# Kernel tuning notes

Measured on AMD Instinct MI355X. Metric: run time of the kernel, lower is better.

## Reference

```python
import jax, jax.numpy as jnp
import numpy as np
from functools import partial

B, T, F_DIM, H_ATT = 1024, 32, 64, 64
NUM_FILTERS, KH, KW = 64, 2, 2
CATE_SIZES = [1665, 217, 2501]  # cate_unique_num + 1
CATE_DIM = 8
NUM_CLASSES = 2
FLAT_DIM = NUM_FILTERS * (T - KH + 1) * (2 * F_DIM - KW + 1)  # 64*31*127
LIN1_IN = FLAT_DIM + 3 * CATE_DIM


def setup_inputs() -> dict:
    key = jax.random.key(0)
    ks = jax.random.split(key, 16)
    X_nume = jax.random.normal(ks[0], (B, T, F_DIM), dtype=jnp.float32)
    X_cate = jax.random.randint(ks[1], (B, 3), 0, 217, dtype=jnp.int64)
    # attention params: uniform(0,1) as in the torch module
    W_att = jax.random.uniform(ks[2], (F_DIM, H_ATT), dtype=jnp.float32)
    U_att = jax.random.uniform(ks[3], (F_DIM, H_ATT), dtype=jnp.float32)
    V_att = jax.random.uniform(ks[4], (H_ATT, 1), dtype=jnp.float32)
    conv_w = jax.random.normal(ks[5], (NUM_FILTERS, 1, KH, KW), dtype=jnp.float32) * 0.1
    conv_b = jax.random.normal(ks[6], (NUM_FILTERS,), dtype=jnp.float32) * 0.01
    emb0 = jax.random.normal(ks[7], (CATE_SIZES[0], CATE_DIM), dtype=jnp.float32)
    emb1 = jax.random.normal(ks[8], (CATE_SIZES[1], CATE_DIM), dtype=jnp.float32)
    emb2 = jax.random.normal(ks[9], (CATE_SIZES[2], CATE_DIM), dtype=jnp.float32)
    w1 = jax.random.normal(ks[10], (256, LIN1_IN), dtype=jnp.float32) * 0.002
    b1 = jnp.zeros((256,), dtype=jnp.float32)
    w2 = jax.random.normal(ks[11], (32, 256), dtype=jnp.float32) * 0.06
    b2 = jnp.zeros((32,), dtype=jnp.float32)
    w3 = jax.random.normal(ks[12], (NUM_CLASSES, 32), dtype=jnp.float32) * 0.17
    b3 = jnp.zeros((NUM_CLASSES,), dtype=jnp.float32)
    return dict(X_nume=X_nume, X_cate=X_cate, W_att=W_att, U_att=U_att, V_att=V_att,
                conv_w=conv_w, conv_b=conv_b, emb0=emb0, emb1=emb1, emb2=emb2,
                w1=w1, b1=b1, w2=w2, b2=b2, w3=w3, b3=b3)


def _forward(X_nume, X_cate, W_att, U_att, V_att, conv_w, conv_b,
             emb0, emb1, emb2, w1, b1, w2, b2, w3, b3):
    # ---- pairwise additive attention over time (GAT-style) ----
    Xw = jnp.einsum('btf,fh->bth', X_nume, W_att)  # [B,T,H]
    Xu = jnp.einsum('btf,fh->bth', X_nume, U_att)  # [B,T,H]
    h = jnp.tanh(Xw[:, :, None, :] + Xu[:, None, :, :])        # [B,T,T,H]
    e = jnp.einsum('bijh,h->bij', h, V_att[:, 0])              # [B,T,T]
    alpha = jax.nn.softmax(e, axis=2)                          # softmax over j (incl. j==i)
    # c_i = sum_{j != i} alpha_ij * x_j  (self term excluded, NOT renormalized)
    c = jnp.einsum('bij,bjf->bif', alpha, X_nume)
    alpha_diag = jnp.einsum('bii->bi', alpha)
    c = c - alpha_diag[:, :, None] * X_nume                    # [B,T,F]
    inp = jnp.concatenate([X_nume, c], axis=-1)                # [B,T,2F]
    # ---- conv 2d (1 -> num_filters, 2x2, valid) + relu ----
    conv_in = inp[:, None, :, :]                               # [B,1,T,2F]
    y = jax.lax.conv_general_dilated(conv_in, conv_w, (1, 1), 'VALID',
                                     dimension_numbers=('NCHW', 'OIHW', 'NCHW'))
    y = jax.nn.relu(y + conv_b[None, :, None, None])           # [B,64,T-1,2F-1]
    flat = y.reshape(y.shape[0], -1)
    # ---- categorical embeddings ----
    cate = jnp.concatenate([emb0[X_cate[:, 0]], emb1[X_cate[:, 1]], emb2[X_cate[:, 2]]], axis=1)
    x = jnp.concatenate([flat, cate], axis=1)
    # ---- MLP head ----
    x = jax.nn.relu(x @ w1.T + b1)
    x = jax.nn.relu(x @ w2.T + b2)
    return x @ w3.T + b3


def reference(X_nume, X_cate, W_att, U_att, V_att, conv_w, conv_b,
              emb0, emb1, emb2, w1, b1, w2, b2, w3, b3):
    return _forward(X_nume, X_cate, W_att, U_att, V_att, conv_w, conv_b,
                    emb0, emb1, emb2, w1, b1, w2, b2, w3, b3)
```

## Files before the change

### kernel.cpp

```cpp
#include <hip/hip_runtime.h>

typedef unsigned short u16;
typedef unsigned int   u32;
typedef __attribute__((ext_vector_type(4))) float f32x4;
typedef __attribute__((ext_vector_type(8))) short s16x8;
typedef __attribute__((ext_vector_type(4))) unsigned short u16x4;

#define FLATD 251968
#define LIN1  251992
#define K_    251968

__device__ __forceinline__ u16 f2bf(float f) {
  u32 u = __float_as_uint(f);
  u32 r = (u + 0x7fffu + ((u >> 16) & 1u)) >> 16;
  return (u16)r;
}

__global__ __launch_bounds__(256) void k_attn_conv(
    const float* __restrict__ Xn, const float* __restrict__ Wa,
    const float* __restrict__ Ua, const float* __restrict__ Va,
    const float* __restrict__ cw, const float* __restrict__ cb,
    u16* __restrict__ flat)
{
  __shared__ float Xs[32][65];
  __shared__ float Xw[32][65];
  __shared__ float Xu[32][65];
  __shared__ float ev[32][33];
  __shared__ float Vs[64];
  __shared__ float ins[32][132];

  const int b = blockIdx.x;
  const int t = threadIdx.x;
  const float* xb = Xn + (size_t)b * 2048;

  for (int v = t; v < 512; v += 256) {
    float4 x = ((const float4*)xb)[v];
    int row = v >> 4, c4 = (v & 15) << 2;
    Xs[row][c4] = x.x; Xs[row][c4 + 1] = x.y; Xs[row][c4 + 2] = x.z; Xs[row][c4 + 3] = x.w;
  }
  if (t < 64) Vs[t] = Va[t];
  __syncthreads();

  {
    const int h = t & 63, iw = t >> 6;
    float aw[8] = {0,0,0,0,0,0,0,0}, au[8] = {0,0,0,0,0,0,0,0};
    for (int f = 0; f < 64; ++f) {
      float wv_ = Wa[f * 64 + h], uv_ = Ua[f * 64 + h];
#pragma unroll
      for (int s = 0; s < 8; ++s) {
        float x = Xs[iw + 4 * s][f];
        aw[s] = fmaf(x, wv_, aw[s]);
        au[s] = fmaf(x, uv_, au[s]);
      }
    }
#pragma unroll
    for (int s = 0; s < 8; ++s) { Xw[iw + 4 * s][h] = aw[s]; Xu[iw + 4 * s][h] = au[s]; }
  }
  __syncthreads();

  for (int p = t; p < 1024; p += 256) {
    int i = p >> 5, j = p & 31;
    float acc = 0.f;
    for (int h = 0; h < 64; ++h) {
      float s  = Xw[i][h] + Xu[j][h];
      float ex = __expf(2.f * s);
      float th = 1.f - 2.f * __builtin_amdgcn_rcpf(ex + 1.f);
      acc = fmaf(th, Vs[h], acc);
    }
    ev[i][j] = acc;
  }
  __syncthreads();

  {
    int i = t >> 3, g = t & 7;
    float e0 = ev[i][g], e1 = ev[i][g + 8], e2 = ev[i][g + 16], e3 = ev[i][g + 24];
    float m = fmaxf(fmaxf(e0, e1), fmaxf(e2, e3));
    m = fmaxf(m, __shfl_xor(m, 1));
    m = fmaxf(m, __shfl_xor(m, 2));
    m = fmaxf(m, __shfl_xor(m, 4));
    float p0 = __expf(e0 - m), p1 = __expf(e1 - m), p2 = __expf(e2 - m), p3 = __expf(e3 - m);
    float s = p0 + p1 + p2 + p3;
    s += __shfl_xor(s, 1); s += __shfl_xor(s, 2); s += __shfl_xor(s, 4);
    float inv = __builtin_amdgcn_rcpf(s);
    ev[i][g] = p0 * inv; ev[i][g + 8] = p1 * inv; ev[i][g + 16] = p2 * inv; ev[i][g + 24] = p3 * inv;
  }
  __syncthreads();

  for (int p = t; p < 2048; p += 256) {
    int i = p >> 6, f = p & 63;
    float acc = 0.f;
#pragma unroll 8
    for (int j = 0; j < 32; ++j) acc = fmaf(ev[i][j], Xs[j][f], acc);
    acc -= ev[i][i] * Xs[i][f];
    ins[i][f]      = Xs[i][f];
    ins[i][64 + f] = acc;
  }
  __syncthreads();

  const int lane = t & 63, wv = t >> 6;
  u16* fb = flat + (size_t)b * FLATD;
  for (int fblk = 0; fblk < 8; ++fblk) {
    float w00[8], w01[8], w10[8], w11[8], bb[8];
#pragma unroll
    for (int j = 0; j < 8; ++j) {
      int f = fblk * 8 + j;
      w00[j] = cw[f * 4 + 0]; w01[j] = cw[f * 4 + 1];
      w10[j] = cw[f * 4 + 2]; w11[j] = cw[f * 4 + 3];
      bb[j]  = cb[f];
    }
    for (int s = wv; s < 62; s += 4) {
      int r = s >> 1;
      int c = ((s & 1) << 6) + lane;
      if (c < 127) {
        float x0 = ins[r][c],     x1 = ins[r][c + 1];
        float y0 = ins[r + 1][c], y1 = ins[r + 1][c + 1];
        u16* po = fb + (size_t)(fblk * 8) * 3937 + r * 127 + c;
#pragma unroll
        for (int j = 0; j < 8; ++j) {
          float y = fmaf(x0, w00[j], fmaf(x1, w01[j],
                    fmaf(y0, w10[j], fmaf(y1, w11[j], bb[j]))));
          po[(size_t)j * 3937] = f2bf(fmaxf(y, 0.f));
        }
      }
    }
  }
}

__global__ __launch_bounds__(256) void k_cast_w1(const float* __restrict__ w1,
                                                 u16* __restrict__ w1b)
{
  const int o = blockIdx.x;
  const int part = blockIdx.y;
  const int t = threadIdx.x;
  const float4* src = (const float4*)(w1 + (size_t)o * LIN1) + part * 7874;
  u16x4* dst = (u16x4*)(w1b + (size_t)o * K_) + part * 7874;
  for (int i = t; i < 7874; i += 256) {
    float4 v = src[i];
    u16x4 o4;
    o4.x = f2bf(v.x); o4.y = f2bf(v.y); o4.z = f2bf(v.z); o4.w = f2bf(v.w);
    dst[i] = o4;
  }
}

__global__ __launch_bounds__(256) void k_cate(
    const int* __restrict__ Xc, const float* __restrict__ e0,
    const float* __restrict__ e1, const float* __restrict__ e2,
    const float* __restrict__ w1, const float* __restrict__ b1,
    float* __restrict__ x1)
{
  __shared__ float es[24];
  const int b = blockIdx.x, t = threadIdx.x;
  if (t < 24) {
    int g = t >> 3, d = t & 7;
    int idx = Xc[b * 3 + g];
    const float* tab = (g == 0) ? e0 : (g == 1) ? e1 : e2;
    es[t] = tab[idx * 8 + d];
  }
  __syncthreads();
  float acc = b1[t];
  const float* wt = w1 + (size_t)t * LIN1 + FLATD;
#pragma unroll
  for (int j = 0; j < 24; ++j) acc = fmaf(es[j], wt[j], acc);
  x1[b * 256 + t] = acc;
}

#define AS1 __attribute__((address_space(1)))
#define AS3 __attribute__((address_space(3)))
__device__ __forceinline__ void g2l16(const void* g, void* l) {
  __builtin_amdgcn_global_load_lds((const AS1 u32*)g, (AS3 u32*)l, 16, 0, 0);
}

__global__ __launch_bounds__(256, 3) void k_gemm(
    const u16* __restrict__ A, const u16* __restrict__ Bw, float* __restrict__ C)
{
  __shared__ u16 As[128 * 32];
  __shared__ u16 Bs[128 * 32];
  const int tile = blockIdx.x;
  const int kc   = blockIdx.y;
  const int mt = tile & 7, nt = tile >> 3;
  const int tid = threadIdx.x;
  const int lane = tid & 63, w = tid >> 6;
  const int wm = w >> 1, wn = w & 1;

  const size_t kbase = (size_t)kc * 4064;
  const u16* gA = A  + ((size_t)(mt * 128 + w * 32 + (lane >> 2))) * K_ + kbase + (size_t)(lane & 3) * 8;
  const u16* gB = Bw + ((size_t)(nt * 128 + w * 32 + (lane >> 2))) * K_ + kbase + (size_t)(lane & 3) * 8;
  char* lA = (char*)As + w * 2048;
  char* lB = (char*)Bs + w * 2048;

  f32x4 acc[4][4] = {};

  const int aoff = (wm * 64 + (lane & 15)) * 64 + (lane >> 4) * 16;
  const int boff = (wn * 64 + (lane & 15)) * 64 + (lane >> 4) * 16;

  for (int ks = 0; ks < 127; ++ks) {
    const size_t ko = (size_t)ks * 32;
    g2l16(gA + ko,                    lA);
    g2l16(gA + ko + (size_t)16 * K_,  lA + 1024);
    g2l16(gB + ko,                    lB);
    g2l16(gB + ko + (size_t)16 * K_,  lB + 1024);
    __syncthreads();
    s16x8 af[4], bf[4];
#pragma unroll
    for (int mi = 0; mi < 4; ++mi)
      af[mi] = *(const s16x8*)((const char*)As + aoff + mi * 1024);
#pragma unroll
    for (int ni = 0; ni < 4; ++ni)
      bf[ni] = *(const s16x8*)((const char*)Bs + boff + ni * 1024);
#pragma unroll
    for (int mi = 0; mi < 4; ++mi)
#pragma unroll
      for (int ni = 0; ni < 4; ++ni)
        acc[mi][ni] = __builtin_amdgcn_mfma_f32_16x16x32_bf16(af[mi], bf[ni], acc[mi][ni], 0, 0, 0);
    __syncthreads();
  }

  const int m0 = mt * 128 + wm * 64 + ((lane >> 4) << 2);
  const int n0 = nt * 128 + wn * 64 + (lane & 15);
#pragma unroll
  for (int mi = 0; mi < 4; ++mi)
#pragma unroll
    for (int ni = 0; ni < 4; ++ni)
#pragma unroll
      for (int r = 0; r < 4; ++r)
        atomicAdd(C + (size_t)(m0 + mi * 16 + r) * 256 + (n0 + ni * 16), acc[mi][ni][r]);
}

__global__ __launch_bounds__(64) void k_tail(
    const float* __restrict__ x1, const float* __restrict__ w2, const float* __restrict__ b2,
    const float* __restrict__ w3, const float* __restrict__ b3, float* __restrict__ out)
{
  __shared__ float x2s[32];
  const int b = blockIdx.x, l = threadIdx.x;
  const int j = l & 31, og = l >> 5;
  const float* xb = x1 + b * 256 + og * 128;
  const float* wr = w2 + j * 256 + og * 128;
  float acc = 0.f;
#pragma unroll 4
  for (int i = 0; i < 128; ++i)
    acc = fmaf(fmaxf(xb[i], 0.f), wr[i], acc);
  acc += __shfl_xor(acc, 32);
  if (og == 0) x2s[j] = fmaxf(acc + b2[j], 0.f);
  __syncthreads();
  if (l < 2) {
    float r = b3[l];
#pragma unroll
    for (int q = 0; q < 32; ++q) r = fmaf(x2s[q], w3[l * 32 + q], r);
    out[(size_t)b * 2 + l] = r;
  }
}

extern "C" void kernel_launch(void* const* d_in, const int* in_sizes, int n_in,
                              void* d_out, int out_size, void* d_ws, size_t ws_size,
                              hipStream_t stream)
{
  const float* Xn = (const float*)d_in[0];
  const int*   Xc = (const int*)d_in[1];
  const float* Wa = (const float*)d_in[2];
  const float* Ua = (const float*)d_in[3];
  const float* Va = (const float*)d_in[4];
  const float* cw = (const float*)d_in[5];
  const float* cb = (const float*)d_in[6];
  const float* e0 = (const float*)d_in[7];
  const float* e1 = (const float*)d_in[8];
  const float* e2 = (const float*)d_in[9];
  const float* w1 = (const float*)d_in[10];
  const float* b1 = (const float*)d_in[11];
  const float* w2 = (const float*)d_in[12];
  const float* b2 = (const float*)d_in[13];
  const float* w3 = (const float*)d_in[14];
  const float* b3 = (const float*)d_in[15];
  float* out = (float*)d_out;

  char* ws = (char*)d_ws;
  u16*   flat = (u16*)ws;
  u16*   w1b  = (u16*)(ws + 516030464ull);
  float* x1   = (float*)(ws + 645038080ull);
  if (ws_size < 646086656ull) return;

  k_attn_conv<<<dim3(1024), dim3(256), 0, stream>>>(Xn, Wa, Ua, Va, cw, cb, flat);
  k_cast_w1 <<<dim3(256, 8), dim3(256), 0, stream>>>(w1, w1b);
  k_cate    <<<dim3(1024), dim3(256), 0, stream>>>(Xc, e0, e1, e2, w1, b1, x1);
  k_gemm    <<<dim3(16, 62), dim3(256), 0, stream>>>(flat, w1b, x1);
  k_tail    <<<dim3(1024), dim3(64), 0, stream>>>(x1, w2, b2, w3, b3, out);
}
```

Baseline: 1.028 ms.

## Double-buffer split-K GEMM with 128x256 tiles and 512-thread blocks

The split-K GEMM now computes a full 128x256 output tile per block with 8 waves, so each A tile is loaded once instead of twice. It uses a two-stage LDS double buffer with explicit vmcnt waits so the next global-to-LDS load overlaps the MFMA work. The split-K factor also goes from 62 to 127 chunks of 1984. The intent is to cut redundant A traffic and hide load latency, at the cost of more atomic adds into the output and a larger LDS footprint per block.

```diff
diff --git a/kernel.cpp b/kernel.cpp
--- a/kernel.cpp
+++ b/kernel.cpp
@@ -170,53 +170,73 @@
   __builtin_amdgcn_global_load_lds((const AS1 u32*)g, (AS3 u32*)l, 16, 0, 0);
 }
 
-__global__ __launch_bounds__(256, 3) void k_gemm(
+__global__ __launch_bounds__(512, 4) void k_gemm(
     const u16* __restrict__ A, const u16* __restrict__ Bw, float* __restrict__ C)
 {
-  __shared__ u16 As[128 * 32];
-  __shared__ u16 Bs[128 * 32];
-  const int tile = blockIdx.x;
-  const int kc   = blockIdx.y;
-  const int mt = tile & 7, nt = tile >> 3;
+  __shared__ u16 lds[2][12288];
+  const int mt = blockIdx.x;
+  const int kc = blockIdx.y;
   const int tid = threadIdx.x;
   const int lane = tid & 63, w = tid >> 6;
-  const int wm = w >> 1, wn = w & 1;
-
-  const size_t kbase = (size_t)kc * 4064;
-  const u16* gA = A  + ((size_t)(mt * 128 + w * 32 + (lane >> 2))) * K_ + kbase + (size_t)(lane & 3) * 8;
-  const u16* gB = Bw + ((size_t)(nt * 128 + w * 32 + (lane >> 2))) * K_ + kbase + (size_t)(lane & 3) * 8;
-  char* lA = (char*)As + w * 2048;
-  char* lB = (char*)Bs + w * 2048;
+  const int wm = w >> 2, wn = w & 3;
+
+  const size_t kbase = (size_t)kc * 1984;
+  const u16* gA  = A  + ((size_t)(mt * 128 + w * 16 + (lane >> 2))) * K_ + kbase + (size_t)(lane & 3) * 8;
+  const u16* gB0 = Bw + ((size_t)(w * 32      + (lane >> 2))) * K_ + kbase + (size_t)(lane & 3) * 8;
+  const u16* gB1 = Bw + ((size_t)(w * 32 + 16 + (lane >> 2))) * K_ + kbase + (size_t)(lane & 3) * 8;
 
   f32x4 acc[4][4] = {};
 
   const int aoff = (wm * 64 + (lane & 15)) * 64 + (lane >> 4) * 16;
-  const int boff = (wn * 64 + (lane & 15)) * 64 + (lane >> 4) * 16;
-
-  for (int ks = 0; ks < 127; ++ks) {
-    const size_t ko = (size_t)ks * 32;
-    g2l16(gA + ko,                    lA);
-    g2l16(gA + ko + (size_t)16 * K_,  lA + 1024);
-    g2l16(gB + ko,                    lB);
-    g2l16(gB + ko + (size_t)16 * K_,  lB + 1024);
-    __syncthreads();
-    s16x8 af[4], bf[4];
-#pragma unroll
-    for (int mi = 0; mi < 4; ++mi)
-      af[mi] = *(const s16x8*)((const char*)As + aoff + mi * 1024);
-#pragma unroll
-    for (int ni = 0; ni < 4; ++ni)
-      bf[ni] = *(const s16x8*)((const char*)Bs + boff + ni * 1024);
-#pragma unroll
-    for (int mi = 0; mi < 4; ++mi)
-#pragma unroll
-      for (int ni = 0; ni < 4; ++ni)
-        acc[mi][ni] = __builtin_amdgcn_mfma_f32_16x16x32_bf16(af[mi], bf[ni], acc[mi][ni], 0, 0, 0);
-    __syncthreads();
-  }
+  const int boff = 8192 + (wn * 64 + (lane & 15)) * 64 + (lane >> 4) * 16;
+
+#define STAGE(T, R)                                                         \
+  {                                                                         \
+    const size_t ko = (size_t)(T) * 32;                                     \
+    char* base = (char*)&lds[R][0];                                         \
+    g2l16(gA  + ko, base + w * 1024);                                       \
+    g2l16(gB0 + ko, base + 8192 + (2 * w) * 1024);                          \
+    g2l16(gB1 + ko, base + 8192 + (2 * w + 1) * 1024);                      \
+  }
+
+#define COMPUTE(R)                                                          \
+  {                                                                         \
+    const char* base = (const char*)&lds[R][0];                             \
+    s16x8 af[4], bf[4];                                                     \
+    _Pragma("unroll")                                                       \
+    for (int mi = 0; mi < 4; ++mi) af[mi] = *(const s16x8*)(base + aoff + mi * 1024); \
+    _Pragma("unroll")                                                       \
+    for (int ni = 0; ni < 4; ++ni) bf[ni] = *(const s16x8*)(base + boff + ni * 1024); \
+    _Pragma("unroll")                                                       \
+    for (int mi = 0; mi < 4; ++mi)                                          \
+      _Pragma("unroll")                                                     \
+      for (int ni = 0; ni < 4; ++ni)                                        \
+        acc[mi][ni] = __builtin_amdgcn_mfma_f32_16x16x32_bf16(af[mi], bf[ni], acc[mi][ni], 0, 0, 0); \
+  }
+
+  STAGE(0, 0);
+  for (int t = 0; t < 61; ++t) {
+    STAGE(t + 1, (t + 1) & 1);
+    asm volatile("s_waitcnt vmcnt(3)" ::: "memory");
+    __builtin_amdgcn_sched_barrier(0);
+    __builtin_amdgcn_s_barrier();
+    asm volatile("" ::: "memory");
+    COMPUTE(t & 1);
+    asm volatile("" ::: "memory");
+    __builtin_amdgcn_s_barrier();
+    asm volatile("" ::: "memory");
+  }
+  asm volatile("s_waitcnt vmcnt(0)" ::: "memory");
+  __builtin_amdgcn_sched_barrier(0);
+  __builtin_amdgcn_s_barrier();
+  asm volatile("" ::: "memory");
+  COMPUTE(1);
+
+#undef STAGE
+#undef COMPUTE
 
   const int m0 = mt * 128 + wm * 64 + ((lane >> 4) << 2);
-  const int n0 = nt * 128 + wn * 64 + (lane & 15);
+  const int n0 = wn * 64 + (lane & 15);
 #pragma unroll
   for (int mi = 0; mi < 4; ++mi)
 #pragma unroll
@@ -281,6 +301,6 @@
   k_attn_conv<<<dim3(1024), dim3(256), 0, stream>>>(Xn, Wa, Ua, Va, cw, cb, flat);
   k_cast_w1 <<<dim3(256, 8), dim3(256), 0, stream>>>(w1, w1b);
   k_cate    <<<dim3(1024), dim3(256), 0, stream>>>(Xc, e0, e1, e2, w1, b1, x1);
-  k_gemm    <<<dim3(16, 62), dim3(256), 0, stream>>>(flat, w1b, x1);
+  k_gemm    <<<dim3(8, 127), dim3(512), 0, stream>>>(flat, w1b, x1);
   k_tail    <<<dim3(1024), dim3(64), 0, stream>>>(x1, w2, b2, w3, b3, out);
 }
```

After: 887.0 us. -13.7%, faster.
